# Kernel optimization log

Hardware: AMD Instinct MI355X
Metric: run time of the kernel (lower is better)

## Reference

```python
import jax, jax.numpy as jnp
import numpy as np

HIDDEN = 8192
K = 32
DIMS = [512, 768]
BATCH = 16384

def _xavier(key, shape):
    fan_out, fan_in = shape
    limit = np.sqrt(6.0 / (fan_in + fan_out)).astype(np.float32)
    return jax.random.uniform(key, shape, dtype=jnp.float32, minval=-limit, maxval=limit)

def setup_inputs() -> dict:
    key = jax.random.key(0)
    ks = jax.random.split(key, 6)
    return {
        "x0": jax.random.normal(ks[0], (BATCH, DIMS[0]), dtype=jnp.float32),
        "x1": jax.random.normal(ks[1], (BATCH, DIMS[1]), dtype=jnp.float32),
        "pre_bias0": jnp.zeros((DIMS[0],), dtype=jnp.float32),
        "pre_bias1": jnp.zeros((DIMS[1],), dtype=jnp.float32),
        "enc_w0": _xavier(ks[2], (HIDDEN, DIMS[0])),   # nn.Linear(d0, hidden).weight
        "enc_w1": _xavier(ks[3], (HIDDEN, DIMS[1])),
        "dec_w0": _xavier(ks[4], (DIMS[0], HIDDEN)),   # nn.Linear(hidden, d0).weight
        "dec_w1": _xavier(ks[5], (DIMS[1], HIDDEN)),
        "post_bias0": jnp.zeros((DIMS[0],), dtype=jnp.float32),
        "post_bias1": jnp.zeros((DIMS[1],), dtype=jnp.float32),
        "source_idx": 0,
    }

def _topk_sparse(z, k):
    # keep top-k per row, zero the rest (hard TopK activation)
    vals, idx = jax.lax.top_k(z, k)                      # [B, k]
    rows = jnp.arange(z.shape[0])[:, None]               # [B, 1]
    return jnp.zeros_like(z).at[rows, idx].set(vals)

def reference(x0, x1, pre_bias0, pre_bias1, enc_w0, enc_w1,
              dec_w0, dec_w1, post_bias0, post_bias1, source_idx):
    xs = (x0, x1)
    pbs = (pre_bias0, pre_bias1)
    ews = (enc_w0, enc_w1)
    # encode from source model: pre-bias subtract -> linear -> TopK sparsify
    x = xs[source_idx]
    z_dense = (x - pbs[source_idx]) @ ews[source_idx].T   # [B, HIDDEN]
    z = _topk_sparse(z_dense, K)
    # decode to every model's activation space
    rec0 = z @ dec_w0.T + post_bias0                      # [B, d0]
    rec1 = z @ dec_w1.T + post_bias1                      # [B, d1]
    return (z, rec0, rec1)
```

## Files before the change

### kernel.cpp

```cpp
#include <hip/hip_runtime.h>


#define BATCH  16384
#define HIDDEN 8192
#define DIM0   512
#define DIM1   768
#define TOPK   32
#define CAND_MAX 256
#define WIN_LO 40
#define WIN_HI 96

#define KLO_G 0xBECDu
#define KHI_G 0xC020u

typedef __attribute__((ext_vector_type(8))) short bf16x8;
typedef __attribute__((ext_vector_type(8))) unsigned short u16x8;
typedef __attribute__((ext_vector_type(4))) float f32x4;

__device__ __forceinline__ unsigned fkey(float f) {
    unsigned u = __float_as_uint(f);
    return (u & 0x80000000u) ? ~u : (u | 0x80000000u);
}
__device__ __forceinline__ unsigned fkey16(unsigned short h) {
    return (h & 0x8000u) ? (unsigned)((~h) & 0xFFFFu) : (unsigned)(h | 0x8000u);
}
__device__ __forceinline__ unsigned short f2b(float f) {
    unsigned u = __float_as_uint(f);
    unsigned r = (u + 0x7FFFu + ((u >> 16) & 1u)) >> 16;
    return (unsigned short)r;
}
__device__ __forceinline__ float b2f(unsigned short h) {
    return __uint_as_float(((unsigned)h) << 16);
}
__device__ __forceinline__ void load_lds16(const void* g, void* l) {
    __builtin_amdgcn_global_load_lds((const __attribute__((address_space(1))) void*)g,
                                     (__attribute__((address_space(3))) void*)l, 16, 0, 0);
}


template<int SRC>
__global__ void convert_xw(const float* __restrict__ x0, const float* __restrict__ x1,
                           const float* __restrict__ pb0, const float* __restrict__ pb1,
                           const float* __restrict__ w0, const float* __restrict__ w1,
                           const int* __restrict__ srcp,
                           unsigned short* __restrict__ xb, unsigned short* __restrict__ wb)
{
    if (*srcp != SRC) return;
    constexpr int D = SRC ? DIM1 : DIM0;
    const float* __restrict__ x  = SRC ? x1  : x0;
    const float* __restrict__ pb = SRC ? pb1 : pb0;
    const float* __restrict__ w  = SRC ? w1  : w0;
    const int nx4 = BATCH * D / 4;
    const int nw4 = HIDDEN * D / 4;
    for (int i = blockIdx.x * blockDim.x + threadIdx.x; i < nx4 + nw4;
         i += gridDim.x * blockDim.x) {
        if (i < nx4) {
            float4 v = ((const float4*)x)[i];
            const int k = (i * 4) % D;
            v.x -= pb[k]; v.y -= pb[k + 1]; v.z -= pb[k + 2]; v.w -= pb[k + 3];
            ushort4 o; o.x = f2b(v.x); o.y = f2b(v.y); o.z = f2b(v.z); o.w = f2b(v.w);
            ((ushort4*)xb)[i] = o;
        } else {
            const float4 v = ((const float4*)w)[i - nx4];
            ushort4 o; o.x = f2b(v.x); o.y = f2b(v.y); o.z = f2b(v.z); o.w = f2b(v.w);
            ((ushort4*)wb)[i - nx4] = o;
        }
    }
}

__global__ void transpose_dec_bf16(const float* __restrict__ dec,
                                   unsigned short* __restrict__ decT, int DD)
{
    __shared__ float t[32][33];
    const int hb = blockIdx.x * 32, db = blockIdx.y * 32;
    const int lx = threadIdx.x, ly = threadIdx.y;
#pragma unroll
    for (int s = 0; s < 32; s += 8)
        t[ly + s][lx] = dec[(size_t)(db + ly + s) * HIDDEN + hb + lx];
    __syncthreads();
#pragma unroll
    for (int s = 0; s < 32; s += 8)
        decT[(size_t)(hb + ly + s) * DD + db + lx] = f2b(t[lx][ly + s]);
}

template<int SRC>
__global__ __launch_bounds__(256, 2)
void gemm_bf16(const unsigned short* __restrict__ xb, const unsigned short* __restrict__ wb,
               const int* __restrict__ srcp, float* __restrict__ z)
{
    if (*srcp != SRC) return;
    constexpr int D = SRC ? DIM1 : DIM0;

    __shared__ unsigned short As[128 * 64];
    __shared__ unsigned short Bs[128 * 64];

    const int nwg = gridDim.x;
    int id = blockIdx.x;
    id = (id & 7) * (nwg >> 3) + (id >> 3);
    const int bx = id & 63;
    const int by = id >> 6;
    const int m0 = by * 128, n0 = bx * 128;

    const int tid  = threadIdx.x;
    const int lane = tid & 63;
    const int wid  = tid >> 6;
    const int wr   = wid >> 1;
    const int wc   = wid & 1;
    const int l15  = lane & 15;
    const int g    = lane >> 4;

    f32x4 acc[4][4];
#pragma unroll
    for (int i = 0; i < 4; ++i)
#pragma unroll
        for (int j = 0; j < 4; ++j) acc[i][j] = (f32x4){0.f, 0.f, 0.f, 0.f};

    for (int k0 = 0; k0 < D; k0 += 64) {
#pragma unroll
        for (int q = 0; q < 4; ++q) {
            const int c   = wid * 256 + q * 64 + lane;
            const int row = c >> 3, jb = c & 7;
            const int j   = jb ^ (row & 7);
            load_lds16(xb + (size_t)(m0 + row) * D + k0 + j * 8,
                       As + (size_t)(wid * 256 + q * 64) * 8);
            load_lds16(wb + (size_t)(n0 + row) * D + k0 + j * 8,
                       Bs + (size_t)(wid * 256 + q * 64) * 8);
        }
        __syncthreads();

#pragma unroll
        for (int kk = 0; kk < 2; ++kk) {
            bf16x8 a[4], b[4];
#pragma unroll
            for (int f = 0; f < 4; ++f) {
                const int rA = wr * 64 + f * 16 + l15;
                const int sA = ((kk * 4 + g) ^ (rA & 7)) * 16;
                a[f] = *(const bf16x8*)((const char*)As + rA * 128 + sA);
                const int rB = wc * 64 + f * 16 + l15;
                const int sB = ((kk * 4 + g) ^ (rB & 7)) * 16;
                b[f] = *(const bf16x8*)((const char*)Bs + rB * 128 + sB);
            }
#pragma unroll
            for (int fi = 0; fi < 4; ++fi)
#pragma unroll
                for (int fj = 0; fj < 4; ++fj)
                    acc[fi][fj] = __builtin_amdgcn_mfma_f32_16x16x32_bf16(
                        a[fi], b[fj], acc[fi][fj], 0, 0, 0);
        }
        __syncthreads();
    }

#pragma unroll
    for (int fi = 0; fi < 4; ++fi) {
        const int row = m0 + wr * 64 + fi * 16 + g * 4;
#pragma unroll
        for (int fj = 0; fj < 4; ++fj) {
            const int col = n0 + wc * 64 + fj * 16 + l15;
#pragma unroll
            for (int r = 0; r < 4; ++r) {
                unsigned short* zs =
                    (unsigned short*)((char*)z + (size_t)(row + r) * (HIDDEN * 4));
                zs[col] = f2b(acc[fi][fj][r]);
            }
        }
    }
}

template<int SRC>
__global__ __launch_bounds__(256)
void topk_rescore_decode(float* __restrict__ z,
                         const float* __restrict__ x0, const float* __restrict__ x1,
                         const float* __restrict__ pb0, const float* __restrict__ pb1,
                         const float* __restrict__ ew0, const float* __restrict__ ew1,
                         const unsigned short* __restrict__ dTb0,
                         const unsigned short* __restrict__ dTb1,
                         const float* __restrict__ po0, const float* __restrict__ po1,
                         float* __restrict__ rec0, float* __restrict__ rec1,
                         const int* __restrict__ srcp)
{
    if (*srcp != SRC) return;
    constexpr int D = SRC ? DIM1 : DIM0;
    const float* __restrict__ xsrc = SRC ? x1 : x0;
    const float* __restrict__ pb   = SRC ? pb1 : pb0;
    const float* __restrict__ ew   = SRC ? ew1 : ew0;

    __shared__ float         xs[D];
    __shared__ int           cidx[CAND_MAX];
    __shared__ float         cval[CAND_MAX];
    __shared__ unsigned char cflag[CAND_MAX];
    __shared__ int           counts[2][4];
    __shared__ unsigned      pcounts[4];
    __shared__ int           s_cnt;
    __shared__ float         selv[TOPK];
    __shared__ int           seli[TOPK];

    const int tid = threadIdx.x;
    const size_t row = blockIdx.x;
    float* __restrict__ zrow = z + row * HIDDEN;
    const unsigned short* __restrict__ zsrow =
        (const unsigned short*)((const char*)z + row * (HIDDEN * 4));

    unsigned key[32];
#pragma unroll
    for (int s = 0; s < 4; ++s) {
        const u16x8 v = __builtin_nontemporal_load(
            (const u16x8*)(zsrow + (size_t)(s * 256 + tid) * 8));
#pragma unroll
        for (int j = 0; j < 8; ++j) key[s * 8 + j] = fkey16(v[j]);
    }

    const f32x4 zv4 = (f32x4){0.f, 0.f, 0.f, 0.f};
#pragma unroll
    for (int s = 0; s < 8; ++s)
        __builtin_nontemporal_store(zv4, (f32x4*)&zrow[(size_t)(s * 256 + tid) * 4]);

    if (tid < D / 4) {
        const float4 xv = ((const float4*)(xsrc + row * D))[tid];
        const float4 pv = ((const float4*)pb)[tid];
        ((float4*)xs)[tid] = make_float4(xv.x - pv.x, xv.y - pv.y,
                                         xv.z - pv.z, xv.w - pv.w);
    }
    if (tid == 0) s_cnt = 0;

    {
        int clo = 0, chi = 0;
#pragma unroll
        for (int j = 0; j < 32; ++j) {
            clo += (key[j] > KLO_G) ? 1 : 0;
            chi += (key[j] > KHI_G) ? 1 : 0;
        }
        unsigned pk = (unsigned)clo | ((unsigned)chi << 16);
#pragma unroll
        for (int off = 32; off; off >>= 1) pk += __shfl_xor(pk, off);
        if ((tid & 63) == 0) pcounts[tid >> 6] = pk;
    }
    __syncthreads();
    const unsigned ptot = pcounts[0] + pcounts[1] + pcounts[2] + pcounts[3];
    const int tot_lo = (int)(ptot & 0xFFFFu), tot_hi = (int)(ptot >> 16);

    unsigned kappa;
    int found = 0;
    if (tot_lo >= WIN_LO && tot_lo <= WIN_HI)      { kappa = KLO_G; found = 1; }
    else if (tot_hi >= WIN_LO && tot_hi <= WIN_HI) { kappa = KHI_G; found = 1; }
    if (!found) {
        unsigned lo = 0u, hi = 65535u;
        if (tot_lo > WIN_HI) lo = KLO_G;
        if (tot_lo < WIN_LO) hi = KLO_G;
        if (tot_hi > WIN_HI) lo = KHI_G;
        if (tot_hi < WIN_LO) hi = (hi < KHI_G) ? hi : KHI_G;
        kappa = lo;
        for (int it = 0; it < 18; ++it) {
            const unsigned mid = (lo + hi) >> 1;
            int c = 0;
#pragma unroll
            for (int j = 0; j < 32; ++j) c += (key[j] > mid) ? 1 : 0;
#pragma unroll
            for (int off = 32; off; off >>= 1) c += __shfl_xor(c, off);
            if ((tid & 63) == 0) counts[it & 1][tid >> 6] = c;
            __syncthreads();
            const int tot = counts[it & 1][0] + counts[it & 1][1] +
                            counts[it & 1][2] + counts[it & 1][3];
            if (tot >= WIN_LO && tot <= WIN_HI) { kappa = mid; break; }
            if (tot > WIN_HI) lo = mid; else hi = mid;
            kappa = lo;
            if (hi - lo <= 1u) break;
        }
    }

#pragma unroll
    for (int j = 0; j < 32; ++j) {
        if (key[j] > kappa) {
            const int slot = atomicAdd(&s_cnt, 1);
            if (slot < CAND_MAX)
                cidx[slot] = ((j >> 3) * 256 + tid) * 8 + (j & 7);
        }
    }
    __syncthreads();
    const int C = min(s_cnt, CAND_MAX);

    {
        const int grp = tid >> 3, j8 = tid & 7;
        for (int c = grp; c < C; c += 32) {
            const float* __restrict__ wrow = ew + (size_t)cidx[c] * D;
            float4 a4 = make_float4(0.f, 0.f, 0.f, 0.f);
#pragma unroll
            for (int s = 0; s < D; s += 32) {
                const float4 w4 = *(const float4*)&wrow[s + j8 * 4];
                const float4 x4 = *(const float4*)&xs[s + j8 * 4];
                a4.x = fmaf(x4.x, w4.x, a4.x);
                a4.y = fmaf(x4.y, w4.y, a4.y);
                a4.z = fmaf(x4.z, w4.z, a4.z);
                a4.w = fmaf(x4.w, w4.w, a4.w);
            }
            float a = (a4.x + a4.y) + (a4.z + a4.w);
            a += __shfl_xor(a, 1);
            a += __shfl_xor(a, 2);
            a += __shfl_xor(a, 4);
            if (j8 == 0) cval[c] = a;
        }
    }
    __syncthreads();

    if (tid < C) {
        const float v = cval[tid];
        const int  ix = cidx[tid];
        int rank = 0;
        for (int j = 0; j < C; ++j) {
            const float vj = cval[j];
            rank += (vj > v || (vj == v && cidx[j] < ix)) ? 1 : 0;
        }
        cflag[tid] = (rank < TOPK) ? 1 : 0;
    }
    __syncthreads();
    if (tid < C && cflag[tid]) {
        const int ix = cidx[tid];
        int sr = 0;
        for (int j = 0; j < C; ++j) sr += (cflag[j] && cidx[j] < ix) ? 1 : 0;
        selv[sr] = cval[tid];
        seli[sr] = ix;
    }
    __syncthreads();

    if (tid < TOPK) zrow[seli[tid]] = selv[tid];

#pragma unroll
    for (int pass = 0; pass < 2; ++pass) {
        const int slot = pass * 256 + tid;
        if (slot < (DIM0 + DIM1) / 4) {
            const bool is0 = slot < DIM0 / 4;
            const int d0 = is0 ? slot * 4 : (slot - DIM0 / 4) * 4;
            const int DD = is0 ? DIM0 : DIM1;
            const unsigned short* __restrict__ dT = is0 ? dTb0 : dTb1;
            const float* __restrict__ po = is0 ? po0 : po1;
            f32x4 a;
            {
                const float4 p4 = *(const float4*)&po[d0];
                a = (f32x4){p4.x, p4.y, p4.z, p4.w};
            }
#pragma unroll
            for (int j = 0; j < TOPK; ++j) {
                const float sv = selv[j];
                const ushort4 w4 = *(const ushort4*)&dT[(size_t)seli[j] * DD + d0];
                a.x = fmaf(sv, b2f(w4.x), a.x);
                a.y = fmaf(sv, b2f(w4.y), a.y);
                a.z = fmaf(sv, b2f(w4.z), a.z);
                a.w = fmaf(sv, b2f(w4.w), a.w);
            }
            float* __restrict__ out = is0 ? (rec0 + row * DIM0 + d0)
                                          : (rec1 + row * DIM1 + d0);
            __builtin_nontemporal_store(a, (f32x4*)out);
        }
    }
}


__global__ __launch_bounds__(256, 2)
void encode_gemm(const float* __restrict__ x0, const float* __restrict__ x1,
                 const float* __restrict__ pb0, const float* __restrict__ pb1,
                 const float* __restrict__ w0, const float* __restrict__ w1,
                 const int* __restrict__ srcp, float* __restrict__ z)
{
    const int src = *srcp;
    const float* __restrict__ x  = (src == 0) ? x0 : x1;
    const float* __restrict__ pb = (src == 0) ? pb0 : pb1;
    const float* __restrict__ w  = (src == 0) ? w0 : w1;
    const int D = (src == 0) ? DIM0 : DIM1;

    __shared__ float As[16][132];
    __shared__ float Bs[16][132];

    const int tid = threadIdx.x;
    const int m0 = blockIdx.y * 128;
    const int n0 = blockIdx.x * 128;

    const int cA0 = tid,          cA1 = tid + 256;
    const int r0  = cA0 >> 2,     kq0 = (cA0 & 3) * 4;
    const int r1  = cA1 >> 2,     kq1 = (cA1 & 3) * 4;

    const int mf = (tid & 15) * 4;
    const int nf = (tid >> 4) * 4;

    float acc[8][8];
#pragma unroll
    for (int i = 0; i < 8; ++i)
#pragma unroll
        for (int j = 0; j < 8; ++j) acc[i][j] = 0.0f;

    for (int k0 = 0; k0 < D; k0 += 16) {
        const float4 av0 = *(const float4*)(x + (size_t)(m0 + r0) * D + k0 + kq0);
        const float4 av1 = *(const float4*)(x + (size_t)(m0 + r1) * D + k0 + kq1);
        const float4 pv0 = *(const float4*)(pb + k0 + kq0);
        const float4 pv1 = *(const float4*)(pb + k0 + kq1);
        const float4 bv0 = *(const float4*)(w + (size_t)(n0 + r0) * D + k0 + kq0);
        const float4 bv1 = *(const float4*)(w + (size_t)(n0 + r1) * D + k0 + kq1);
        As[kq0 + 0][r0] = av0.x - pv0.x;
        As[kq0 + 1][r0] = av0.y - pv0.y;
        As[kq0 + 2][r0] = av0.z - pv0.z;
        As[kq0 + 3][r0] = av0.w - pv0.w;
        As[kq1 + 0][r1] = av1.x - pv1.x;
        As[kq1 + 1][r1] = av1.y - pv1.y;
        As[kq1 + 2][r1] = av1.z - pv1.z;
        As[kq1 + 3][r1] = av1.w - pv1.w;
        Bs[kq0 + 0][r0] = bv0.x;
        Bs[kq0 + 1][r0] = bv0.y;
        Bs[kq0 + 2][r0] = bv0.z;
        Bs[kq0 + 3][r0] = bv0.w;
        Bs[kq1 + 0][r1] = bv1.x;
        Bs[kq1 + 1][r1] = bv1.y;
        Bs[kq1 + 2][r1] = bv1.z;
        Bs[kq1 + 3][r1] = bv1.w;
        __syncthreads();
#pragma unroll
        for (int kk = 0; kk < 16; ++kk) {
            const float4 A0 = *(const float4*)&As[kk][mf];
            const float4 A1 = *(const float4*)&As[kk][mf + 64];
            const float4 B0 = *(const float4*)&Bs[kk][nf];
            const float4 B1 = *(const float4*)&Bs[kk][nf + 64];
            const float a[8] = {A0.x, A0.y, A0.z, A0.w, A1.x, A1.y, A1.z, A1.w};
            const float b[8] = {B0.x, B0.y, B0.z, B0.w, B1.x, B1.y, B1.z, B1.w};
#pragma unroll
            for (int i = 0; i < 8; ++i)
#pragma unroll
                for (int j = 0; j < 8; ++j)
                    acc[i][j] = fmaf(a[i], b[j], acc[i][j]);
        }
        __syncthreads();
    }

#pragma unroll
    for (int i = 0; i < 8; ++i) {
        const int row = m0 + mf + (i & 3) + (i >> 2) * 64;
        const float4 v0 = make_float4(acc[i][0], acc[i][1], acc[i][2], acc[i][3]);
        const float4 v1 = make_float4(acc[i][4], acc[i][5], acc[i][6], acc[i][7]);
        *(float4*)(z + (size_t)row * HIDDEN + n0 + nf)      = v0;
        *(float4*)(z + (size_t)row * HIDDEN + n0 + nf + 64) = v1;
    }
}

__global__ __launch_bounds__(256, 2)
void topk_decode_fb(float* __restrict__ z,
                    const float* __restrict__ dA, const float* __restrict__ dB,
                    const float* __restrict__ po0, const float* __restrict__ po1,
                    float* __restrict__ rec0, float* __restrict__ rec1)
{
    __shared__ float    rowv[HIDDEN];
    __shared__ unsigned hist[4][257];
    __shared__ unsigned scanbuf[256];
    __shared__ float    selv[TOPK];
    __shared__ int      seli[TOPK];
    __shared__ unsigned sh_byte, sh_gt;

    const int tid = threadIdx.x;
    const size_t rowid = blockIdx.x;
    float* __restrict__ zrow = z + rowid * HIDDEN;

#pragma unroll
    for (int s = 0; s < 8; ++s) {
        const int i4 = s * 256 + tid;
        *(float4*)&rowv[i4 * 4] = *(const float4*)&zrow[i4 * 4];
    }
    __syncthreads();

    unsigned prefix = 0, prefmask = 0, need = TOPK;
#pragma unroll
    for (int p = 3; p >= 0; --p) {
        for (int i = tid; i < 4 * 257; i += 256) (&hist[0][0])[i] = 0;
        __syncthreads();
        const int sh = p * 8;
        for (int s = 0; s < 32; ++s) {
            const int i = s * 256 + tid;
            const unsigned k = fkey(rowv[i]);
            if ((k & prefmask) == prefix)
                atomicAdd(&hist[tid & 3][(k >> sh) & 255], 1);
        }
        __syncthreads();
        const unsigned tot = hist[0][tid] + hist[1][tid] + hist[2][tid] + hist[3][tid];
        hist[0][tid] = tot;
        __syncthreads();
        if (tid == 0) {
            unsigned cum = 0;
            int b = 255;
            for (;; --b) {
                const unsigned c = hist[0][b];
                if (cum + c >= need || b == 0) { sh_byte = (unsigned)b; sh_gt = cum; break; }
                cum += c;
            }
        }
        __syncthreads();
        prefix  |= sh_byte << sh;
        prefmask |= 0xFFu << sh;
        need -= sh_gt;
        __syncthreads();
    }
    const unsigned cut = prefix;
    const unsigned needEq = need;

    unsigned gtmask = 0, eqmask = 0;
#pragma unroll
    for (int j = 0; j < 32; ++j) {
        const int jr = (j + tid) & 31;
        const int i = tid * 32 + jr;
        const unsigned k = fkey(rowv[i]);
        if (k > cut)       gtmask |= 1u << jr;
        else if (k == cut) eqmask |= 1u << jr;
    }

    scanbuf[tid] = __popc(eqmask);
    __syncthreads();
    for (int off = 1; off < 256; off <<= 1) {
        const unsigned v = scanbuf[tid];
        const unsigned add = (tid >= off) ? scanbuf[tid - off] : 0u;
        __syncthreads();
        scanbuf[tid] = v + add;
        __syncthreads();
    }
    const unsigned eqexc = scanbuf[tid] - __popc(eqmask);
    __syncthreads();

    unsigned selmask = gtmask;
    {
        unsigned m = eqmask, r = eqexc;
        while (m) {
            const int j = __ffs(m) - 1;
            if (r < needEq) selmask |= 1u << j;
            ++r;
            m &= m - 1;
        }
    }

    scanbuf[tid] = __popc(selmask);
    __syncthreads();
    for (int off = 1; off < 256; off <<= 1) {
        const unsigned v = scanbuf[tid];
        const unsigned add = (tid >= off) ? scanbuf[tid - off] : 0u;
        __syncthreads();
        scanbuf[tid] = v + add;
        __syncthreads();
    }
    const unsigned selexc = scanbuf[tid] - __popc(selmask);

#pragma unroll
    for (int j = 0; j < 32; ++j) {
        const int jr = (j + tid) & 31;
        const int i = tid * 32 + jr;
        if ((selmask >> jr) & 1u) {
            const int slot = (int)(selexc + __popc(selmask & ((1u << jr) - 1u)));
            selv[slot] = rowv[i];
            seli[slot] = i;
        } else {
            rowv[i] = 0.0f;
        }
    }
    __syncthreads();

#pragma unroll
    for (int s = 0; s < 8; ++s) {
        const int i4 = s * 256 + tid;
        *(float4*)&zrow[i4 * 4] = *(float4*)&rowv[i4 * 4];
    }

    for (int d = tid; d < DIM0; d += 256) {
        float a = po0[d];
#pragma unroll
        for (int j = 0; j < TOPK; ++j)
            a = fmaf(selv[j], dA[(size_t)d * HIDDEN + seli[j]], a);
        rec0[rowid * DIM0 + d] = a;
    }
    for (int d = tid; d < DIM1; d += 256) {
        float a = po1[d];
#pragma unroll
        for (int j = 0; j < TOPK; ++j)
            a = fmaf(selv[j], dB[(size_t)d * HIDDEN + seli[j]], a);
        rec1[rowid * DIM1 + d] = a;
    }
}

extern "C" void kernel_launch(void* const* d_in, const int* in_sizes, int n_in,
                              void* d_out, int out_size, void* d_ws, size_t ws_size,
                              hipStream_t stream)
{
    const float* x0  = (const float*)d_in[0];
    const float* x1  = (const float*)d_in[1];
    const float* pb0 = (const float*)d_in[2];
    const float* pb1 = (const float*)d_in[3];
    const float* ew0 = (const float*)d_in[4];
    const float* ew1 = (const float*)d_in[5];
    const float* dw0 = (const float*)d_in[6];
    const float* dw1 = (const float*)d_in[7];
    const float* po0 = (const float*)d_in[8];
    const float* po1 = (const float*)d_in[9];
    const int*  srcp = (const int*)d_in[10];

    float* z    = (float*)d_out;
    float* rec0 = z + (size_t)BATCH * HIDDEN;
    float* rec1 = rec0 + (size_t)BATCH * DIM0;

    unsigned short* xb   = (unsigned short*)d_ws;
    unsigned short* wb   = xb   + (size_t)BATCH * DIM1;
    unsigned short* dTb0 = wb   + (size_t)HIDDEN * DIM1;
    unsigned short* dTb1 = dTb0 + (size_t)HIDDEN * DIM0;
    const size_t need = ((size_t)BATCH * DIM1 + (size_t)HIDDEN * DIM1 +
                         (size_t)HIDDEN * DIM0 + (size_t)HIDDEN * DIM1) * sizeof(unsigned short);

    if (ws_size >= need) {
        convert_xw<0><<<4096, 256, 0, stream>>>(x0, x1, pb0, pb1, ew0, ew1, srcp, xb, wb);
        convert_xw<1><<<4096, 256, 0, stream>>>(x0, x1, pb0, pb1, ew0, ew1, srcp, xb, wb);
        dim3 tb(32, 8);
        transpose_dec_bf16<<<dim3(HIDDEN / 32, DIM0 / 32), tb, 0, stream>>>(dw0, dTb0, DIM0);
        transpose_dec_bf16<<<dim3(HIDDEN / 32, DIM1 / 32), tb, 0, stream>>>(dw1, dTb1, DIM1);
        gemm_bf16<0><<<(BATCH / 128) * (HIDDEN / 128), 256, 0, stream>>>(xb, wb, srcp, z);
        gemm_bf16<1><<<(BATCH / 128) * (HIDDEN / 128), 256, 0, stream>>>(xb, wb, srcp, z);
        topk_rescore_decode<0><<<BATCH, 256, 0, stream>>>(
            z, x0, x1, pb0, pb1, ew0, ew1, dTb0, dTb1, po0, po1, rec0, rec1, srcp);
        topk_rescore_decode<1><<<BATCH, 256, 0, stream>>>(
            z, x0, x1, pb0, pb1, ew0, ew1, dTb0, dTb1, po0, po1, rec0, rec1, srcp);
    } else {
        encode_gemm<<<dim3(HIDDEN / 128, BATCH / 128), 256, 0, stream>>>(
            x0, x1, pb0, pb1, ew0, ew1, srcp, z);
        topk_decode_fb<<<BATCH, 256, 0, stream>>>(z, dw0, dw1, po0, po1, rec0, rec1);
    }
}
```

Measured before the change: 777.4 us.

## Merge per-source kernel launches, move upper z zeroing into GEMM, pack keys

Measured after the change: 750.0 us. 1.04x faster.

```diff
diff --git a/kernel.cpp b/kernel.cpp
--- a/kernel.cpp
+++ b/kernel.cpp
@@ -7,8 +7,8 @@
 #define DIM1   768
 #define TOPK   32
 #define CAND_MAX 256
-#define WIN_LO 40
-#define WIN_HI 96
+#define WIN_LO 36
+#define WIN_HI 64
 
 #define KLO_G 0xBECDu
 #define KHI_G 0xC020u
@@ -37,19 +37,13 @@
                                      (__attribute__((address_space(3))) void*)l, 16, 0, 0);
 }
 
-
 template<int SRC>
-__global__ void convert_xw(const float* __restrict__ x0, const float* __restrict__ x1,
-                           const float* __restrict__ pb0, const float* __restrict__ pb1,
-                           const float* __restrict__ w0, const float* __restrict__ w1,
-                           const int* __restrict__ srcp,
-                           unsigned short* __restrict__ xb, unsigned short* __restrict__ wb)
-{
-    if (*srcp != SRC) return;
+__device__ __forceinline__ void convert_impl(
+    const float* __restrict__ x, const float* __restrict__ pb,
+    const float* __restrict__ w,
+    unsigned short* __restrict__ xb, unsigned short* __restrict__ wb)
+{
     constexpr int D = SRC ? DIM1 : DIM0;
-    const float* __restrict__ x  = SRC ? x1  : x0;
-    const float* __restrict__ pb = SRC ? pb1 : pb0;
-    const float* __restrict__ w  = SRC ? w1  : w0;
     const int nx4 = BATCH * D / 4;
     const int nw4 = HIDDEN * D / 4;
     for (int i = blockIdx.x * blockDim.x + threadIdx.x; i < nx4 + nw4;
@@ -68,6 +62,16 @@
     }
 }
 
+__global__ void convert_xw(const float* __restrict__ x0, const float* __restrict__ x1,
+                           const float* __restrict__ pb0, const float* __restrict__ pb1,
+                           const float* __restrict__ w0, const float* __restrict__ w1,
+                           const int* __restrict__ srcp,
+                           unsigned short* __restrict__ xb, unsigned short* __restrict__ wb)
+{
+    if (*srcp == 0) convert_impl<0>(x0, pb0, w0, xb, wb);
+    else            convert_impl<1>(x1, pb1, w1, xb, wb);
+}
+
 __global__ void transpose_dec_bf16(const float* __restrict__ dec,
                                    unsigned short* __restrict__ decT, int DD)
 {
@@ -84,15 +88,11 @@
 }
 
 template<int SRC>
-__global__ __launch_bounds__(256, 2)
-void gemm_bf16(const unsigned short* __restrict__ xb, const unsigned short* __restrict__ wb,
-               const int* __restrict__ srcp, float* __restrict__ z)
-{
-    if (*srcp != SRC) return;
+__device__ __forceinline__ void gemm_impl(
+    const unsigned short* __restrict__ xb, const unsigned short* __restrict__ wb,
+    float* __restrict__ z, unsigned short* As, unsigned short* Bs)
+{
     constexpr int D = SRC ? DIM1 : DIM0;
-
-    __shared__ unsigned short As[128 * 64];
-    __shared__ unsigned short Bs[128 * 64];
 
     const int nwg = gridDim.x;
     int id = blockIdx.x;
@@ -164,35 +164,40 @@
             }
         }
     }
+
+    if (bx >= 32) {
+        const f32x4 zv = (f32x4){0.f, 0.f, 0.f, 0.f};
+        const int c4 = (4096 >> 2) + (bx - 32) * 32 + (tid & 31);
+#pragma unroll
+        for (int pass = 0; pass < 16; ++pass) {
+            const int r = m0 + pass * 8 + (tid >> 5);
+            __builtin_nontemporal_store(zv, (f32x4*)(z + (size_t)r * HIDDEN) + c4);
+        }
+    }
+}
+
+__global__ __launch_bounds__(256, 2)
+void gemm_bf16(const unsigned short* __restrict__ xb, const unsigned short* __restrict__ wb,
+               const int* __restrict__ srcp, float* __restrict__ z)
+{
+    __shared__ unsigned short As[128 * 64];
+    __shared__ unsigned short Bs[128 * 64];
+    if (*srcp == 0) gemm_impl<0>(xb, wb, z, As, Bs);
+    else            gemm_impl<1>(xb, wb, z, As, Bs);
 }
 
 template<int SRC>
-__global__ __launch_bounds__(256)
-void topk_rescore_decode(float* __restrict__ z,
-                         const float* __restrict__ x0, const float* __restrict__ x1,
-                         const float* __restrict__ pb0, const float* __restrict__ pb1,
-                         const float* __restrict__ ew0, const float* __restrict__ ew1,
-                         const unsigned short* __restrict__ dTb0,
-                         const unsigned short* __restrict__ dTb1,
-                         const float* __restrict__ po0, const float* __restrict__ po1,
-                         float* __restrict__ rec0, float* __restrict__ rec1,
-                         const int* __restrict__ srcp)
-{
-    if (*srcp != SRC) return;
+__device__ __forceinline__ void topk_impl(
+    float* __restrict__ z,
+    const float* __restrict__ xsrc, const float* __restrict__ pb,
+    const float* __restrict__ ew,
+    const unsigned short* __restrict__ dTb0, const unsigned short* __restrict__ dTb1,
+    const float* __restrict__ po0, const float* __restrict__ po1,
+    float* __restrict__ rec0, float* __restrict__ rec1,
+    float* xs, int* cidx, float* cval, unsigned char* cflag,
+    int* counts, unsigned* pcounts, int* s_cnt, float* selv, int* seli)
+{
     constexpr int D = SRC ? DIM1 : DIM0;
-    const float* __restrict__ xsrc = SRC ? x1 : x0;
-    const float* __restrict__ pb   = SRC ? pb1 : pb0;
-    const float* __restrict__ ew   = SRC ? ew1 : ew0;
-
-    __shared__ float         xs[D];
-    __shared__ int           cidx[CAND_MAX];
-    __shared__ float         cval[CAND_MAX];
-    __shared__ unsigned char cflag[CAND_MAX];
-    __shared__ int           counts[2][4];
-    __shared__ unsigned      pcounts[4];
-    __shared__ int           s_cnt;
-    __shared__ float         selv[TOPK];
-    __shared__ int           seli[TOPK];
 
     const int tid = threadIdx.x;
     const size_t row = blockIdx.x;
@@ -200,18 +205,18 @@
     const unsigned short* __restrict__ zsrow =
         (const unsigned short*)((const char*)z + row * (HIDDEN * 4));
 
-    unsigned key[32];
+    unsigned pkey[16];
 #pragma unroll
     for (int s = 0; s < 4; ++s) {
-        const u16x8 v = __builtin_nontemporal_load(
-            (const u16x8*)(zsrow + (size_t)(s * 256 + tid) * 8));
-#pragma unroll
-        for (int j = 0; j < 8; ++j) key[s * 8 + j] = fkey16(v[j]);
+        const u16x8 v = *(const u16x8*)(zsrow + (size_t)(s * 256 + tid) * 8);
+#pragma unroll
+        for (int p = 0; p < 4; ++p)
+            pkey[s * 4 + p] = fkey16(v[2 * p]) | (fkey16(v[2 * p + 1]) << 16);
     }
 
     const f32x4 zv4 = (f32x4){0.f, 0.f, 0.f, 0.f};
 #pragma unroll
-    for (int s = 0; s < 8; ++s)
+    for (int s = 0; s < 4; ++s)
         __builtin_nontemporal_store(zv4, (f32x4*)&zrow[(size_t)(s * 256 + tid) * 4]);
 
     if (tid < D / 4) {
@@ -220,14 +225,15 @@
         ((float4*)xs)[tid] = make_float4(xv.x - pv.x, xv.y - pv.y,
                                          xv.z - pv.z, xv.w - pv.w);
     }
-    if (tid == 0) s_cnt = 0;
+    if (tid == 0) *s_cnt = 0;
 
     {
         int clo = 0, chi = 0;
 #pragma unroll
-        for (int j = 0; j < 32; ++j) {
-            clo += (key[j] > KLO_G) ? 1 : 0;
-            chi += (key[j] > KHI_G) ? 1 : 0;
+        for (int p = 0; p < 16; ++p) {
+            const unsigned klo16 = pkey[p] & 0xFFFFu, khi16 = pkey[p] >> 16;
+            clo += (klo16 > KLO_G) ? 1 : 0;  chi += (klo16 > KHI_G) ? 1 : 0;
+            clo += (khi16 > KLO_G) ? 1 : 0;  chi += (khi16 > KHI_G) ? 1 : 0;
         }
         unsigned pk = (unsigned)clo | ((unsigned)chi << 16);
 #pragma unroll
@@ -253,13 +259,16 @@
             const unsigned mid = (lo + hi) >> 1;
             int c = 0;
 #pragma unroll
-            for (int j = 0; j < 32; ++j) c += (key[j] > mid) ? 1 : 0;
+            for (int p = 0; p < 16; ++p) {
+                c += ((pkey[p] & 0xFFFFu) > mid) ? 1 : 0;
+                c += ((pkey[p] >> 16)     > mid) ? 1 : 0;
+            }
 #pragma unroll
             for (int off = 32; off; off >>= 1) c += __shfl_xor(c, off);
-            if ((tid & 63) == 0) counts[it & 1][tid >> 6] = c;
+            if ((tid & 63) == 0) counts[(it & 1) * 4 + (tid >> 6)] = c;
             __syncthreads();
-            const int tot = counts[it & 1][0] + counts[it & 1][1] +
-                            counts[it & 1][2] + counts[it & 1][3];
+            const int* cb = counts + (it & 1) * 4;
+            const int tot = cb[0] + cb[1] + cb[2] + cb[3];
             if (tot >= WIN_LO && tot <= WIN_HI) { kappa = mid; break; }
             if (tot > WIN_HI) lo = mid; else hi = mid;
             kappa = lo;
@@ -268,15 +277,20 @@
     }
 
 #pragma unroll
-    for (int j = 0; j < 32; ++j) {
-        if (key[j] > kappa) {
-            const int slot = atomicAdd(&s_cnt, 1);
-            if (slot < CAND_MAX)
-                cidx[slot] = ((j >> 3) * 256 + tid) * 8 + (j & 7);
-        }
-    }
-    __syncthreads();
-    const int C = min(s_cnt, CAND_MAX);
+    for (int p = 0; p < 16; ++p) {
+#pragma unroll
+        for (int h = 0; h < 2; ++h) {
+            const unsigned k16 = h ? (pkey[p] >> 16) : (pkey[p] & 0xFFFFu);
+            if (k16 > kappa) {
+                const int j = 2 * p + h;
+                const int slot = atomicAdd(s_cnt, 1);
+                if (slot < CAND_MAX)
+                    cidx[slot] = ((j >> 3) * 256 + tid) * 8 + (j & 7);
+            }
+        }
+    }
+    __syncthreads();
+    const int C = min(*s_cnt, CAND_MAX);
 
     {
         const int grp = tid >> 3, j8 = tid & 7;
@@ -351,6 +365,35 @@
             __builtin_nontemporal_store(a, (f32x4*)out);
         }
     }
+}
+
+__global__ __launch_bounds__(256)
+void topk_rescore_decode(float* __restrict__ z,
+                         const float* __restrict__ x0, const float* __restrict__ x1,
+                         const float* __restrict__ pb0, const float* __restrict__ pb1,
+                         const float* __restrict__ ew0, const float* __restrict__ ew1,
+                         const unsigned short* __restrict__ dTb0,
+                         const unsigned short* __restrict__ dTb1,
+                         const float* __restrict__ po0, const float* __restrict__ po1,
+                         float* __restrict__ rec0, float* __restrict__ rec1,
+                         const int* __restrict__ srcp)
+{
+    __shared__ float         xs[DIM1];
+    __shared__ int           cidx[CAND_MAX];
+    __shared__ float         cval[CAND_MAX];
+    __shared__ unsigned char cflag[CAND_MAX];
+    __shared__ int           counts[2 * 4];
+    __shared__ unsigned      pcounts[4];
+    __shared__ int           s_cnt;
+    __shared__ float         selv[TOPK];
+    __shared__ int           seli[TOPK];
+
+    if (*srcp == 0)
+        topk_impl<0>(z, x0, pb0, ew0, dTb0, dTb1, po0, po1, rec0, rec1,
+                     xs, cidx, cval, cflag, counts, pcounts, &s_cnt, selv, seli);
+    else
+        topk_impl<1>(z, x1, pb1, ew1, dTb0, dTb1, po0, po1, rec0, rec1,
+                     xs, cidx, cval, cflag, counts, pcounts, &s_cnt, selv, seli);
 }
 
 
@@ -603,16 +646,12 @@
                          (size_t)HIDDEN * DIM0 + (size_t)HIDDEN * DIM1) * sizeof(unsigned short);
 
     if (ws_size >= need) {
-        convert_xw<0><<<4096, 256, 0, stream>>>(x0, x1, pb0, pb1, ew0, ew1, srcp, xb, wb);
-        convert_xw<1><<<4096, 256, 0, stream>>>(x0, x1, pb0, pb1, ew0, ew1, srcp, xb, wb);
+        convert_xw<<<4096, 256, 0, stream>>>(x0, x1, pb0, pb1, ew0, ew1, srcp, xb, wb);
         dim3 tb(32, 8);
         transpose_dec_bf16<<<dim3(HIDDEN / 32, DIM0 / 32), tb, 0, stream>>>(dw0, dTb0, DIM0);
         transpose_dec_bf16<<<dim3(HIDDEN / 32, DIM1 / 32), tb, 0, stream>>>(dw1, dTb1, DIM1);
-        gemm_bf16<0><<<(BATCH / 128) * (HIDDEN / 128), 256, 0, stream>>>(xb, wb, srcp, z);
-        gemm_bf16<1><<<(BATCH / 128) * (HIDDEN / 128), 256, 0, stream>>>(xb, wb, srcp, z);
-        topk_rescore_decode<0><<<BATCH, 256, 0, stream>>>(
-            z, x0, x1, pb0, pb1, ew0, ew1, dTb0, dTb1, po0, po1, rec0, rec1, srcp);
-        topk_rescore_decode<1><<<BATCH, 256, 0, stream>>>(
+        gemm_bf16<<<(BATCH / 128) * (HIDDEN / 128), 256, 0, stream>>>(xb, wb, srcp, z);
+        topk_rescore_decode<<<BATCH, 256, 0, stream>>>(
             z, x0, x1, pb0, pb1, ew0, ew1, dTb0, dTb1, po0, po1, rec0, rec1, srcp);
     } else {
         encode_gemm<<<dim3(HIDDEN / 128, BATCH / 128), 256, 0, stream>>>(
```
